# Kernel optimization log

Measured on AMD Instinct MI355X. Metric: run time of the kernel, lower is better.

## Reference

```python
import jax, jax.numpy as jnp
import numpy as np


def setup_inputs() -> dict:
    key = jax.random.key(0)
    k1, = jax.random.split(key, 1)
    b, l, h, w, c = 2, 16, 16, 16, 32
    inputs = jax.random.normal(k1, (b, l, h, w, c), dtype=jnp.float32)
    gamma = jnp.ones((1,), dtype=jnp.float32)
    return {"inputs": inputs, "gamma": gamma}


def reference(inputs, gamma):
    b, l, h, w, c = inputs.shape
    n = l * h * w
    # torch: x = permute->view gives [b, c, n]; here keep [b, n, c] (same memory layout of values)
    xr = inputs.reshape(b, n, c)
    # scores[b,i,j] = sum_c x[b,c,i] * x[b,c,j]
    scores = jnp.einsum('bic,bjc->bij', xr, xr)
    attn = jax.nn.softmax(scores, axis=-1)  # softmax over j (dim=-1)
    # out[b,c,j] = sum_i x[b,c,i] * attn[b,i,j]  ->  [b, n, c] layout
    out = jnp.einsum('bic,bij->bjc', xr, attn)
    out = out.reshape(b, l, h, w, c)
    return out * gamma + inputs
```

## Files before the change

### kernel.cpp

```cpp
#include <hip/hip_runtime.h>


typedef _Float16 half8 __attribute__((ext_vector_type(8)));
typedef _Float16 half4v __attribute__((ext_vector_type(4)));
typedef _Float16 half2v __attribute__((ext_vector_type(2)));
typedef float float4v __attribute__((ext_vector_type(4)));
typedef int int4v __attribute__((ext_vector_type(4)));

#define NN 4096
#define CC 32
#define L2E 1.44269504f
#define SHIFT 48.0f

__global__ __launch_bounds__(256) void k_convert(const float* __restrict__ x,
                                                 _Float16* __restrict__ xf,
                                                 _Float16* __restrict__ xt) {
    const int t = blockIdx.x * 256 + threadIdx.x;
    const int n  = t & 4095;
    const int cg = (t >> 12) & 7;
    const int b  = t >> 15;
    const int row = (b << 12) | n;
    const float4* src = (const float4*)(x + (size_t)row * CC + cg * 4);
    float4 v = *src;
    _Float16 h0 = (_Float16)v.x, h1 = (_Float16)v.y, h2 = (_Float16)v.z, h3 = (_Float16)v.w;
    *(half4v*)(xf + (size_t)row * CC + cg * 4) = (half4v){h0, h1, h2, h3};
    _Float16* xtb = xt + (size_t)b * CC * NN;
    xtb[(cg * 4 + 0) * NN + n] = h0;
    xtb[(cg * 4 + 1) * NN + n] = h1;
    xtb[(cg * 4 + 2) * NN + n] = h2;
    xtb[(cg * 4 + 3) * NN + n] = h3;
}

__global__ __launch_bounds__(512, 2) void k_pass1(const _Float16* __restrict__ xf,
                                                  float* __restrict__ c2out) {
    const int tid = threadIdx.x;
    const int wave = tid >> 6, lane = tid & 63;
    const int quad = lane >> 4, l15 = lane & 15;
    const int b = blockIdx.x >> 7;
    const int i0 = (blockIdx.x & 127) * 32;
    const _Float16* xb = xf + (size_t)b * NN * CC;

    const half8 af0 = *(const half8*)(xb + (size_t)(i0 + l15) * CC + quad * 8);
    const half8 af1 = *(const half8*)(xb + (size_t)(i0 + 16 + l15) * CC + quad * 8);
    const float4v zf = {0.f, 0.f, 0.f, 0.f};
    float z0[4] = {0.f, 0.f, 0.f, 0.f};
    float z1[4] = {0.f, 0.f, 0.f, 0.f};
    const float c2c = -SHIFT * L2E;

    const int jbase = wave * 512;
    half8 b0 = *(const half8*)(xb + (size_t)(jbase + l15) * CC + quad * 8);
    half8 b1 = *(const half8*)(xb + (size_t)(jbase + 16 + l15) * CC + quad * 8);
    half8 b2 = *(const half8*)(xb + (size_t)(jbase + 32 + l15) * CC + quad * 8);
    half8 b3 = *(const half8*)(xb + (size_t)(jbase + 48 + l15) * CC + quad * 8);

    for (int jt = 0; jt < 8; ++jt) {
        const int jn = jbase + ((jt + 1) & 7) * 64;
        half8 n0 = *(const half8*)(xb + (size_t)(jn + l15) * CC + quad * 8);
        half8 n1 = *(const half8*)(xb + (size_t)(jn + 16 + l15) * CC + quad * 8);
        half8 n2 = *(const half8*)(xb + (size_t)(jn + 32 + l15) * CC + quad * 8);
        half8 n3 = *(const half8*)(xb + (size_t)(jn + 48 + l15) * CC + quad * 8);

        float4v s00 = __builtin_amdgcn_mfma_f32_16x16x32_f16(af0, b0, zf, 0, 0, 0);
        float4v s01 = __builtin_amdgcn_mfma_f32_16x16x32_f16(af0, b1, zf, 0, 0, 0);
        float4v s02 = __builtin_amdgcn_mfma_f32_16x16x32_f16(af0, b2, zf, 0, 0, 0);
        float4v s03 = __builtin_amdgcn_mfma_f32_16x16x32_f16(af0, b3, zf, 0, 0, 0);
        float4v s10 = __builtin_amdgcn_mfma_f32_16x16x32_f16(af1, b0, zf, 0, 0, 0);
        float4v s11 = __builtin_amdgcn_mfma_f32_16x16x32_f16(af1, b1, zf, 0, 0, 0);
        float4v s12 = __builtin_amdgcn_mfma_f32_16x16x32_f16(af1, b2, zf, 0, 0, 0);
        float4v s13 = __builtin_amdgcn_mfma_f32_16x16x32_f16(af1, b3, zf, 0, 0, 0);
#pragma unroll
        for (int r = 0; r < 4; ++r) {
            z0[r] += __builtin_amdgcn_exp2f(fmaf(s00[r], L2E, c2c));
            z0[r] += __builtin_amdgcn_exp2f(fmaf(s01[r], L2E, c2c));
            z0[r] += __builtin_amdgcn_exp2f(fmaf(s02[r], L2E, c2c));
            z0[r] += __builtin_amdgcn_exp2f(fmaf(s03[r], L2E, c2c));
            z1[r] += __builtin_amdgcn_exp2f(fmaf(s10[r], L2E, c2c));
            z1[r] += __builtin_amdgcn_exp2f(fmaf(s11[r], L2E, c2c));
            z1[r] += __builtin_amdgcn_exp2f(fmaf(s12[r], L2E, c2c));
            z1[r] += __builtin_amdgcn_exp2f(fmaf(s13[r], L2E, c2c));
        }
        b0 = n0; b1 = n1; b2 = n2; b3 = n3;
    }
#pragma unroll
    for (int off = 1; off <= 8; off <<= 1) {
#pragma unroll
        for (int r = 0; r < 4; ++r) {
            z0[r] += __shfl_xor(z0[r], off, 64);
            z1[r] += __shfl_xor(z1[r], off, 64);
        }
    }
    __shared__ float zw[8][32];
    if (l15 == 0) {
#pragma unroll
        for (int r = 0; r < 4; ++r) {
            zw[wave][quad * 4 + r]      = z0[r];
            zw[wave][16 + quad * 4 + r] = z1[r];
        }
    }
    __syncthreads();
    if (tid < 32) {
        float zs = 0.f;
#pragma unroll
        for (int w = 0; w < 8; ++w) zs += zw[w][tid];
        c2out[b * NN + i0 + tid] = -(__builtin_amdgcn_logf(zs) + SHIFT * L2E);
    }
}

__global__ __launch_bounds__(512, 2) void k_pass2(const _Float16* __restrict__ xf,
                                                  const _Float16* __restrict__ xt,
                                                  const float* __restrict__ c2,
                                                  const float* __restrict__ x,
                                                  const float* __restrict__ gamma,
                                                  float* __restrict__ out) {
    const int tid = threadIdx.x;
    const int wave = tid >> 6, lane = tid & 63;
    const int quad = lane >> 4, l15 = lane & 15;
    const int b = blockIdx.x >> 7;
    const int j0 = (blockIdx.x & 127) * 32;
    const _Float16* xb  = xf + (size_t)b * NN * CC;
    const _Float16* xtb = xt + (size_t)b * CC * NN;
    const float* c2b = c2 + b * NN;

    __shared__ float red[8][32][32];

    const int addrLo = (((quad & 1) << 5) + l15) << 2;
    const int addrHi = addrLo + 64;
    const bool lo32 = (lane < 32);

    const half8 bj0 = *(const half8*)(xb + (size_t)(j0 + l15) * CC + quad * 8);
    const half8 bj1 = *(const half8*)(xb + (size_t)(j0 + 16 + l15) * CC + quad * 8);
    const float4v zf = {0.f, 0.f, 0.f, 0.f};
    float4v acc00 = zf, acc01 = zf, acc10 = zf, acc11 = zf;

    const int ibase = wave * 512;
    half8 a0  = *(const half8*)(xb + (size_t)(ibase + l15) * CC + quad * 8);
    half8 a1  = *(const half8*)(xb + (size_t)(ibase + 16 + l15) * CC + quad * 8);
    half8 xb0 = *(const half8*)(xtb + (size_t)l15 * NN + ibase + quad * 8);
    half8 xb1 = *(const half8*)(xtb + (size_t)(l15 + 16) * NN + ibase + quad * 8);
    float4v c20 = *(const float4v*)(c2b + ibase + quad * 4);
    float4v c21 = *(const float4v*)(c2b + ibase + 16 + quad * 4);

    for (int it = 0; it < 16; ++it) {
        const int inx = ibase + ((it + 1) & 15) * 32;
        half8 na0  = *(const half8*)(xb + (size_t)(inx + l15) * CC + quad * 8);
        half8 na1  = *(const half8*)(xb + (size_t)(inx + 16 + l15) * CC + quad * 8);
        half8 nxb0 = *(const half8*)(xtb + (size_t)l15 * NN + inx + quad * 8);
        half8 nxb1 = *(const half8*)(xtb + (size_t)(l15 + 16) * NN + inx + quad * 8);
        float4v nc20 = *(const float4v*)(c2b + inx + quad * 4);
        float4v nc21 = *(const float4v*)(c2b + inx + 16 + quad * 4);

        float4v s00 = __builtin_amdgcn_mfma_f32_16x16x32_f16(a0, bj0, zf, 0, 0, 0);
        float4v s10 = __builtin_amdgcn_mfma_f32_16x16x32_f16(a1, bj0, zf, 0, 0, 0);
        float4v s01 = __builtin_amdgcn_mfma_f32_16x16x32_f16(a0, bj1, zf, 0, 0, 0);
        float4v s11 = __builtin_amdgcn_mfma_f32_16x16x32_f16(a1, bj1, zf, 0, 0, 0);
        float4v e00, e10, e01, e11;
#pragma unroll
        for (int r = 0; r < 4; ++r) {
            e00[r] = __builtin_amdgcn_exp2f(fmaf(s00[r], L2E, c20[r]));
            e10[r] = __builtin_amdgcn_exp2f(fmaf(s10[r], L2E, c21[r]));
            e01[r] = __builtin_amdgcn_exp2f(fmaf(s01[r], L2E, c20[r]));
            e11[r] = __builtin_amdgcn_exp2f(fmaf(s11[r], L2E, c21[r]));
        }
        {
            const int d0 = __builtin_bit_cast(int, (half2v)__builtin_amdgcn_cvt_pkrtz(e00[0], e00[1]));
            const int d1 = __builtin_bit_cast(int, (half2v)__builtin_amdgcn_cvt_pkrtz(e00[2], e00[3]));
            const int d2 = __builtin_bit_cast(int, (half2v)__builtin_amdgcn_cvt_pkrtz(e10[0], e10[1]));
            const int d3 = __builtin_bit_cast(int, (half2v)__builtin_amdgcn_cvt_pkrtz(e10[2], e10[3]));
            const int q0 = __builtin_amdgcn_ds_bpermute(addrLo, d0);
            const int q1 = __builtin_amdgcn_ds_bpermute(addrLo, d1);
            const int q2 = __builtin_amdgcn_ds_bpermute(addrHi, d0);
            const int q3 = __builtin_amdgcn_ds_bpermute(addrHi, d1);
            const int q4 = __builtin_amdgcn_ds_bpermute(addrLo, d2);
            const int q5 = __builtin_amdgcn_ds_bpermute(addrLo, d3);
            const int q6 = __builtin_amdgcn_ds_bpermute(addrHi, d2);
            const int q7 = __builtin_amdgcn_ds_bpermute(addrHi, d3);
            int4v ai;
            ai[0] = lo32 ? q0 : q4;
            ai[1] = lo32 ? q1 : q5;
            ai[2] = lo32 ? q2 : q6;
            ai[3] = lo32 ? q3 : q7;
            const half8 a2 = __builtin_bit_cast(half8, ai);
            acc00 = __builtin_amdgcn_mfma_f32_16x16x32_f16(a2, xb0, acc00, 0, 0, 0);
            acc01 = __builtin_amdgcn_mfma_f32_16x16x32_f16(a2, xb1, acc01, 0, 0, 0);
        }
        {
            const int d0 = __builtin_bit_cast(int, (half2v)__builtin_amdgcn_cvt_pkrtz(e01[0], e01[1]));
            const int d1 = __builtin_bit_cast(int, (half2v)__builtin_amdgcn_cvt_pkrtz(e01[2], e01[3]));
            const int d2 = __builtin_bit_cast(int, (half2v)__builtin_amdgcn_cvt_pkrtz(e11[0], e11[1]));
            const int d3 = __builtin_bit_cast(int, (half2v)__builtin_amdgcn_cvt_pkrtz(e11[2], e11[3]));
            const int q0 = __builtin_amdgcn_ds_bpermute(addrLo, d0);
            const int q1 = __builtin_amdgcn_ds_bpermute(addrLo, d1);
            const int q2 = __builtin_amdgcn_ds_bpermute(addrHi, d0);
            const int q3 = __builtin_amdgcn_ds_bpermute(addrHi, d1);
            const int q4 = __builtin_amdgcn_ds_bpermute(addrLo, d2);
            const int q5 = __builtin_amdgcn_ds_bpermute(addrLo, d3);
            const int q6 = __builtin_amdgcn_ds_bpermute(addrHi, d2);
            const int q7 = __builtin_amdgcn_ds_bpermute(addrHi, d3);
            int4v ai;
            ai[0] = lo32 ? q0 : q4;
            ai[1] = lo32 ? q1 : q5;
            ai[2] = lo32 ? q2 : q6;
            ai[3] = lo32 ? q3 : q7;
            const half8 a2 = __builtin_bit_cast(half8, ai);
            acc10 = __builtin_amdgcn_mfma_f32_16x16x32_f16(a2, xb0, acc10, 0, 0, 0);
            acc11 = __builtin_amdgcn_mfma_f32_16x16x32_f16(a2, xb1, acc11, 0, 0, 0);
        }

        a0 = na0; a1 = na1; xb0 = nxb0; xb1 = nxb1; c20 = nc20; c21 = nc21;
    }

#pragma unroll
    for (int r = 0; r < 4; ++r) {
        red[wave][quad * 4 + r][l15]           = acc00[r];
        red[wave][quad * 4 + r][l15 + 16]      = acc01[r];
        red[wave][16 + quad * 4 + r][l15]      = acc10[r];
        red[wave][16 + quad * 4 + r][l15 + 16] = acc11[r];
    }
    __syncthreads();
    {
        const int jj = tid >> 5, c = tid & 31;
        const float g = gamma[0];
#pragma unroll
        for (int h = 0; h < 2; ++h) {
            const int j = jj + h * 16;
            float s = 0.f;
#pragma unroll
            for (int w = 0; w < 8; ++w) s += red[w][j][c];
            const size_t o = (size_t)(b * NN + j0 + j) * CC + c;
            out[o] = fmaf(g, s, x[o]);
        }
    }
}

extern "C" void kernel_launch(void* const* d_in, const int* in_sizes, int n_in,
                              void* d_out, int out_size, void* d_ws, size_t ws_size,
                              hipStream_t stream) {
    const float* x     = (const float*)d_in[0];
    const float* gamma = (const float*)d_in[1];
    float* out = (float*)d_out;

    _Float16* xf = (_Float16*)d_ws;
    _Float16* xt = xf + (size_t)2 * NN * CC;
    float*    c2 = (float*)(xt + (size_t)2 * CC * NN);

    k_convert<<<dim3(256), dim3(256), 0, stream>>>(x, xf, xt);
    k_pass1 <<<dim3(256), dim3(512), 0, stream>>>(xf, c2);
    k_pass2 <<<dim3(256), dim3(512), 0, stream>>>(xf, xt, c2, x, gamma, out);
}
```

Measured before the change: 79.65 us.

## Double per-block query tile to 64 rows and tile transposed copy for contiguous loads

Both attention passes now process 64 rows/columns per block instead of 32, so each loaded key/value fragment is reused across twice as many MFMA tiles, and the grid drops from 256 to 128 blocks. The transposed fp16 copy is re-laid out in 32-position chunks so each lane's 8-element load in pass 2 is contiguous within a small tile rather than strided by N. The trade-off is fewer blocks than compute units on a 256-CU device, more registers and more shared memory (64 KB reduction buffer) per block, which may reduce occupancy.

```diff
diff --git a/kernel.cpp b/kernel.cpp
--- a/kernel.cpp
+++ b/kernel.cpp
@@ -24,11 +24,11 @@
     float4 v = *src;
     _Float16 h0 = (_Float16)v.x, h1 = (_Float16)v.y, h2 = (_Float16)v.z, h3 = (_Float16)v.w;
     *(half4v*)(xf + (size_t)row * CC + cg * 4) = (half4v){h0, h1, h2, h3};
-    _Float16* xtb = xt + (size_t)b * CC * NN;
-    xtb[(cg * 4 + 0) * NN + n] = h0;
-    xtb[(cg * 4 + 1) * NN + n] = h1;
-    xtb[(cg * 4 + 2) * NN + n] = h2;
-    xtb[(cg * 4 + 3) * NN + n] = h3;
+    _Float16* p = xt + (size_t)b * CC * NN + (size_t)(n >> 5) * (CC * 32) + cg * 4 * 32 + (n & 31);
+    p[0]  = h0;
+    p[32] = h1;
+    p[64] = h2;
+    p[96] = h3;
 }
 
 __global__ __launch_bounds__(512, 2) void k_pass1(const _Float16* __restrict__ xf,
@@ -36,15 +36,19 @@
     const int tid = threadIdx.x;
     const int wave = tid >> 6, lane = tid & 63;
     const int quad = lane >> 4, l15 = lane & 15;
-    const int b = blockIdx.x >> 7;
-    const int i0 = (blockIdx.x & 127) * 32;
+    const int b = blockIdx.x >> 6;
+    const int i0 = (blockIdx.x & 63) * 64;
     const _Float16* xb = xf + (size_t)b * NN * CC;
 
     const half8 af0 = *(const half8*)(xb + (size_t)(i0 + l15) * CC + quad * 8);
     const half8 af1 = *(const half8*)(xb + (size_t)(i0 + 16 + l15) * CC + quad * 8);
+    const half8 af2 = *(const half8*)(xb + (size_t)(i0 + 32 + l15) * CC + quad * 8);
+    const half8 af3 = *(const half8*)(xb + (size_t)(i0 + 48 + l15) * CC + quad * 8);
     const float4v zf = {0.f, 0.f, 0.f, 0.f};
     float z0[4] = {0.f, 0.f, 0.f, 0.f};
     float z1[4] = {0.f, 0.f, 0.f, 0.f};
+    float z2[4] = {0.f, 0.f, 0.f, 0.f};
+    float z3[4] = {0.f, 0.f, 0.f, 0.f};
     const float c2c = -SHIFT * L2E;
 
     const int jbase = wave * 512;
@@ -60,24 +64,47 @@
         half8 n2 = *(const half8*)(xb + (size_t)(jn + 32 + l15) * CC + quad * 8);
         half8 n3 = *(const half8*)(xb + (size_t)(jn + 48 + l15) * CC + quad * 8);
 
-        float4v s00 = __builtin_amdgcn_mfma_f32_16x16x32_f16(af0, b0, zf, 0, 0, 0);
-        float4v s01 = __builtin_amdgcn_mfma_f32_16x16x32_f16(af0, b1, zf, 0, 0, 0);
-        float4v s02 = __builtin_amdgcn_mfma_f32_16x16x32_f16(af0, b2, zf, 0, 0, 0);
-        float4v s03 = __builtin_amdgcn_mfma_f32_16x16x32_f16(af0, b3, zf, 0, 0, 0);
-        float4v s10 = __builtin_amdgcn_mfma_f32_16x16x32_f16(af1, b0, zf, 0, 0, 0);
-        float4v s11 = __builtin_amdgcn_mfma_f32_16x16x32_f16(af1, b1, zf, 0, 0, 0);
-        float4v s12 = __builtin_amdgcn_mfma_f32_16x16x32_f16(af1, b2, zf, 0, 0, 0);
-        float4v s13 = __builtin_amdgcn_mfma_f32_16x16x32_f16(af1, b3, zf, 0, 0, 0);
-#pragma unroll
-        for (int r = 0; r < 4; ++r) {
-            z0[r] += __builtin_amdgcn_exp2f(fmaf(s00[r], L2E, c2c));
-            z0[r] += __builtin_amdgcn_exp2f(fmaf(s01[r], L2E, c2c));
-            z0[r] += __builtin_amdgcn_exp2f(fmaf(s02[r], L2E, c2c));
-            z0[r] += __builtin_amdgcn_exp2f(fmaf(s03[r], L2E, c2c));
-            z1[r] += __builtin_amdgcn_exp2f(fmaf(s10[r], L2E, c2c));
-            z1[r] += __builtin_amdgcn_exp2f(fmaf(s11[r], L2E, c2c));
-            z1[r] += __builtin_amdgcn_exp2f(fmaf(s12[r], L2E, c2c));
-            z1[r] += __builtin_amdgcn_exp2f(fmaf(s13[r], L2E, c2c));
+        {
+            float4v s00 = __builtin_amdgcn_mfma_f32_16x16x32_f16(af0, b0, zf, 0, 0, 0);
+            float4v s01 = __builtin_amdgcn_mfma_f32_16x16x32_f16(af0, b1, zf, 0, 0, 0);
+            float4v s02 = __builtin_amdgcn_mfma_f32_16x16x32_f16(af0, b2, zf, 0, 0, 0);
+            float4v s03 = __builtin_amdgcn_mfma_f32_16x16x32_f16(af0, b3, zf, 0, 0, 0);
+            float4v s10 = __builtin_amdgcn_mfma_f32_16x16x32_f16(af1, b0, zf, 0, 0, 0);
+            float4v s11 = __builtin_amdgcn_mfma_f32_16x16x32_f16(af1, b1, zf, 0, 0, 0);
+            float4v s12 = __builtin_amdgcn_mfma_f32_16x16x32_f16(af1, b2, zf, 0, 0, 0);
+            float4v s13 = __builtin_amdgcn_mfma_f32_16x16x32_f16(af1, b3, zf, 0, 0, 0);
+#pragma unroll
+            for (int r = 0; r < 4; ++r) {
+                z0[r] += __builtin_amdgcn_exp2f(fmaf(s00[r], L2E, c2c));
+                z0[r] += __builtin_amdgcn_exp2f(fmaf(s01[r], L2E, c2c));
+                z0[r] += __builtin_amdgcn_exp2f(fmaf(s02[r], L2E, c2c));
+                z0[r] += __builtin_amdgcn_exp2f(fmaf(s03[r], L2E, c2c));
+                z1[r] += __builtin_amdgcn_exp2f(fmaf(s10[r], L2E, c2c));
+                z1[r] += __builtin_amdgcn_exp2f(fmaf(s11[r], L2E, c2c));
+                z1[r] += __builtin_amdgcn_exp2f(fmaf(s12[r], L2E, c2c));
+                z1[r] += __builtin_amdgcn_exp2f(fmaf(s13[r], L2E, c2c));
+            }
+        }
+        {
+            float4v s00 = __builtin_amdgcn_mfma_f32_16x16x32_f16(af2, b0, zf, 0, 0, 0);
+            float4v s01 = __builtin_amdgcn_mfma_f32_16x16x32_f16(af2, b1, zf, 0, 0, 0);
+            float4v s02 = __builtin_amdgcn_mfma_f32_16x16x32_f16(af2, b2, zf, 0, 0, 0);
+            float4v s03 = __builtin_amdgcn_mfma_f32_16x16x32_f16(af2, b3, zf, 0, 0, 0);
+            float4v s10 = __builtin_amdgcn_mfma_f32_16x16x32_f16(af3, b0, zf, 0, 0, 0);
+            float4v s11 = __builtin_amdgcn_mfma_f32_16x16x32_f16(af3, b1, zf, 0, 0, 0);
+            float4v s12 = __builtin_amdgcn_mfma_f32_16x16x32_f16(af3, b2, zf, 0, 0, 0);
+            float4v s13 = __builtin_amdgcn_mfma_f32_16x16x32_f16(af3, b3, zf, 0, 0, 0);
+#pragma unroll
+            for (int r = 0; r < 4; ++r) {
+                z2[r] += __builtin_amdgcn_exp2f(fmaf(s00[r], L2E, c2c));
+                z2[r] += __builtin_amdgcn_exp2f(fmaf(s01[r], L2E, c2c));
+                z2[r] += __builtin_amdgcn_exp2f(fmaf(s02[r], L2E, c2c));
+                z2[r] += __builtin_amdgcn_exp2f(fmaf(s03[r], L2E, c2c));
+                z3[r] += __builtin_amdgcn_exp2f(fmaf(s10[r], L2E, c2c));
+                z3[r] += __builtin_amdgcn_exp2f(fmaf(s11[r], L2E, c2c));
+                z3[r] += __builtin_amdgcn_exp2f(fmaf(s12[r], L2E, c2c));
+                z3[r] += __builtin_amdgcn_exp2f(fmaf(s13[r], L2E, c2c));
+            }
         }
         b0 = n0; b1 = n1; b2 = n2; b3 = n3;
     }
@@ -87,18 +114,22 @@
         for (int r = 0; r < 4; ++r) {
             z0[r] += __shfl_xor(z0[r], off, 64);
             z1[r] += __shfl_xor(z1[r], off, 64);
-        }
-    }
-    __shared__ float zw[8][32];
+            z2[r] += __shfl_xor(z2[r], off, 64);
+            z3[r] += __shfl_xor(z3[r], off, 64);
+        }
+    }
+    __shared__ float zw[8][64];
     if (l15 == 0) {
 #pragma unroll
         for (int r = 0; r < 4; ++r) {
             zw[wave][quad * 4 + r]      = z0[r];
             zw[wave][16 + quad * 4 + r] = z1[r];
+            zw[wave][32 + quad * 4 + r] = z2[r];
+            zw[wave][48 + quad * 4 + r] = z3[r];
         }
     }
     __syncthreads();
-    if (tid < 32) {
+    if (tid < 64) {
         float zs = 0.f;
 #pragma unroll
         for (int w = 0; w < 8; ++w) zs += zw[w][tid];
@@ -115,13 +146,13 @@
     const int tid = threadIdx.x;
     const int wave = tid >> 6, lane = tid & 63;
     const int quad = lane >> 4, l15 = lane & 15;
-    const int b = blockIdx.x >> 7;
-    const int j0 = (blockIdx.x & 127) * 32;
+    const int b = blockIdx.x >> 6;
+    const int j0 = (blockIdx.x & 63) * 64;
     const _Float16* xb  = xf + (size_t)b * NN * CC;
     const _Float16* xtb = xt + (size_t)b * CC * NN;
     const float* c2b = c2 + b * NN;
 
-    __shared__ float red[8][32][32];
+    __shared__ float red[8][64][32];
 
     const int addrLo = (((quad & 1) << 5) + l15) << 2;
     const int addrHi = addrLo + 64;
@@ -129,14 +160,17 @@
 
     const half8 bj0 = *(const half8*)(xb + (size_t)(j0 + l15) * CC + quad * 8);
     const half8 bj1 = *(const half8*)(xb + (size_t)(j0 + 16 + l15) * CC + quad * 8);
+    const half8 bj2 = *(const half8*)(xb + (size_t)(j0 + 32 + l15) * CC + quad * 8);
+    const half8 bj3 = *(const half8*)(xb + (size_t)(j0 + 48 + l15) * CC + quad * 8);
     const float4v zf = {0.f, 0.f, 0.f, 0.f};
     float4v acc00 = zf, acc01 = zf, acc10 = zf, acc11 = zf;
+    float4v acc20 = zf, acc21 = zf, acc30 = zf, acc31 = zf;
 
     const int ibase = wave * 512;
     half8 a0  = *(const half8*)(xb + (size_t)(ibase + l15) * CC + quad * 8);
     half8 a1  = *(const half8*)(xb + (size_t)(ibase + 16 + l15) * CC + quad * 8);
-    half8 xb0 = *(const half8*)(xtb + (size_t)l15 * NN + ibase + quad * 8);
-    half8 xb1 = *(const half8*)(xtb + (size_t)(l15 + 16) * NN + ibase + quad * 8);
+    half8 xb0 = *(const half8*)(xtb + (size_t)ibase * 32 + l15 * 32 + quad * 8);
+    half8 xb1 = *(const half8*)(xtb + (size_t)ibase * 32 + 512 + l15 * 32 + quad * 8);
     float4v c20 = *(const float4v*)(c2b + ibase + quad * 4);
     float4v c21 = *(const float4v*)(c2b + ibase + 16 + quad * 4);
 
@@ -144,66 +178,126 @@
         const int inx = ibase + ((it + 1) & 15) * 32;
         half8 na0  = *(const half8*)(xb + (size_t)(inx + l15) * CC + quad * 8);
         half8 na1  = *(const half8*)(xb + (size_t)(inx + 16 + l15) * CC + quad * 8);
-        half8 nxb0 = *(const half8*)(xtb + (size_t)l15 * NN + inx + quad * 8);
-        half8 nxb1 = *(const half8*)(xtb + (size_t)(l15 + 16) * NN + inx + quad * 8);
+        half8 nxb0 = *(const half8*)(xtb + (size_t)inx * 32 + l15 * 32 + quad * 8);
+        half8 nxb1 = *(const half8*)(xtb + (size_t)inx * 32 + 512 + l15 * 32 + quad * 8);
         float4v nc20 = *(const float4v*)(c2b + inx + quad * 4);
         float4v nc21 = *(const float4v*)(c2b + inx + 16 + quad * 4);
 
-        float4v s00 = __builtin_amdgcn_mfma_f32_16x16x32_f16(a0, bj0, zf, 0, 0, 0);
-        float4v s10 = __builtin_amdgcn_mfma_f32_16x16x32_f16(a1, bj0, zf, 0, 0, 0);
-        float4v s01 = __builtin_amdgcn_mfma_f32_16x16x32_f16(a0, bj1, zf, 0, 0, 0);
-        float4v s11 = __builtin_amdgcn_mfma_f32_16x16x32_f16(a1, bj1, zf, 0, 0, 0);
-        float4v e00, e10, e01, e11;
-#pragma unroll
-        for (int r = 0; r < 4; ++r) {
-            e00[r] = __builtin_amdgcn_exp2f(fmaf(s00[r], L2E, c20[r]));
-            e10[r] = __builtin_amdgcn_exp2f(fmaf(s10[r], L2E, c21[r]));
-            e01[r] = __builtin_amdgcn_exp2f(fmaf(s01[r], L2E, c20[r]));
-            e11[r] = __builtin_amdgcn_exp2f(fmaf(s11[r], L2E, c21[r]));
-        }
         {
-            const int d0 = __builtin_bit_cast(int, (half2v)__builtin_amdgcn_cvt_pkrtz(e00[0], e00[1]));
-            const int d1 = __builtin_bit_cast(int, (half2v)__builtin_amdgcn_cvt_pkrtz(e00[2], e00[3]));
-            const int d2 = __builtin_bit_cast(int, (half2v)__builtin_amdgcn_cvt_pkrtz(e10[0], e10[1]));
-            const int d3 = __builtin_bit_cast(int, (half2v)__builtin_amdgcn_cvt_pkrtz(e10[2], e10[3]));
-            const int q0 = __builtin_amdgcn_ds_bpermute(addrLo, d0);
-            const int q1 = __builtin_amdgcn_ds_bpermute(addrLo, d1);
-            const int q2 = __builtin_amdgcn_ds_bpermute(addrHi, d0);
-            const int q3 = __builtin_amdgcn_ds_bpermute(addrHi, d1);
-            const int q4 = __builtin_amdgcn_ds_bpermute(addrLo, d2);
-            const int q5 = __builtin_amdgcn_ds_bpermute(addrLo, d3);
-            const int q6 = __builtin_amdgcn_ds_bpermute(addrHi, d2);
-            const int q7 = __builtin_amdgcn_ds_bpermute(addrHi, d3);
-            int4v ai;
-            ai[0] = lo32 ? q0 : q4;
-            ai[1] = lo32 ? q1 : q5;
-            ai[2] = lo32 ? q2 : q6;
-            ai[3] = lo32 ? q3 : q7;
-            const half8 a2 = __builtin_bit_cast(half8, ai);
-            acc00 = __builtin_amdgcn_mfma_f32_16x16x32_f16(a2, xb0, acc00, 0, 0, 0);
-            acc01 = __builtin_amdgcn_mfma_f32_16x16x32_f16(a2, xb1, acc01, 0, 0, 0);
+            float4v s00 = __builtin_amdgcn_mfma_f32_16x16x32_f16(a0, bj0, zf, 0, 0, 0);
+            float4v s10 = __builtin_amdgcn_mfma_f32_16x16x32_f16(a1, bj0, zf, 0, 0, 0);
+            float4v s01 = __builtin_amdgcn_mfma_f32_16x16x32_f16(a0, bj1, zf, 0, 0, 0);
+            float4v s11 = __builtin_amdgcn_mfma_f32_16x16x32_f16(a1, bj1, zf, 0, 0, 0);
+            float4v e00, e10, e01, e11;
+#pragma unroll
+            for (int r = 0; r < 4; ++r) {
+                e00[r] = __builtin_amdgcn_exp2f(fmaf(s00[r], L2E, c20[r]));
+                e10[r] = __builtin_amdgcn_exp2f(fmaf(s10[r], L2E, c21[r]));
+                e01[r] = __builtin_amdgcn_exp2f(fmaf(s01[r], L2E, c20[r]));
+                e11[r] = __builtin_amdgcn_exp2f(fmaf(s11[r], L2E, c21[r]));
+            }
+            {
+                const int d0 = __builtin_bit_cast(int, (half2v)__builtin_amdgcn_cvt_pkrtz(e00[0], e00[1]));
+                const int d1 = __builtin_bit_cast(int, (half2v)__builtin_amdgcn_cvt_pkrtz(e00[2], e00[3]));
+                const int d2 = __builtin_bit_cast(int, (half2v)__builtin_amdgcn_cvt_pkrtz(e10[0], e10[1]));
+                const int d3 = __builtin_bit_cast(int, (half2v)__builtin_amdgcn_cvt_pkrtz(e10[2], e10[3]));
+                const int q0 = __builtin_amdgcn_ds_bpermute(addrLo, d0);
+                const int q1 = __builtin_amdgcn_ds_bpermute(addrLo, d1);
+                const int q2 = __builtin_amdgcn_ds_bpermute(addrHi, d0);
+                const int q3 = __builtin_amdgcn_ds_bpermute(addrHi, d1);
+                const int q4 = __builtin_amdgcn_ds_bpermute(addrLo, d2);
+                const int q5 = __builtin_amdgcn_ds_bpermute(addrLo, d3);
+                const int q6 = __builtin_amdgcn_ds_bpermute(addrHi, d2);
+                const int q7 = __builtin_amdgcn_ds_bpermute(addrHi, d3);
+                int4v ai;
+                ai[0] = lo32 ? q0 : q4;
+                ai[1] = lo32 ? q1 : q5;
+                ai[2] = lo32 ? q2 : q6;
+                ai[3] = lo32 ? q3 : q7;
+                const half8 a2 = __builtin_bit_cast(half8, ai);
+                acc00 = __builtin_amdgcn_mfma_f32_16x16x32_f16(a2, xb0, acc00, 0, 0, 0);
+                acc01 = __builtin_amdgcn_mfma_f32_16x16x32_f16(a2, xb1, acc01, 0, 0, 0);
+            }
+            {
+                const int d0 = __builtin_bit_cast(int, (half2v)__builtin_amdgcn_cvt_pkrtz(e01[0], e01[1]));
+                const int d1 = __builtin_bit_cast(int, (half2v)__builtin_amdgcn_cvt_pkrtz(e01[2], e01[3]));
+                const int d2 = __builtin_bit_cast(int, (half2v)__builtin_amdgcn_cvt_pkrtz(e11[0], e11[1]));
+                const int d3 = __builtin_bit_cast(int, (half2v)__builtin_amdgcn_cvt_pkrtz(e11[2], e11[3]));
+                const int q0 = __builtin_amdgcn_ds_bpermute(addrLo, d0);
+                const int q1 = __builtin_amdgcn_ds_bpermute(addrLo, d1);
+                const int q2 = __builtin_amdgcn_ds_bpermute(addrHi, d0);
+                const int q3 = __builtin_amdgcn_ds_bpermute(addrHi, d1);
+                const int q4 = __builtin_amdgcn_ds_bpermute(addrLo, d2);
+                const int q5 = __builtin_amdgcn_ds_bpermute(addrLo, d3);
+                const int q6 = __builtin_amdgcn_ds_bpermute(addrHi, d2);
+                const int q7 = __builtin_amdgcn_ds_bpermute(addrHi, d3);
+                int4v ai;
+                ai[0] = lo32 ? q0 : q4;
+                ai[1] = lo32 ? q1 : q5;
+                ai[2] = lo32 ? q2 : q6;
+                ai[3] = lo32 ? q3 : q7;
+                const half8 a2 = __builtin_bit_cast(half8, ai);
+                acc10 = __builtin_amdgcn_mfma_f32_16x16x32_f16(a2, xb0, acc10, 0, 0, 0);
+                acc11 = __builtin_amdgcn_mfma_f32_16x16x32_f16(a2, xb1, acc11, 0, 0, 0);
+            }
         }
         {
-            const int d0 = __builtin_bit_cast(int, (half2v)__builtin_amdgcn_cvt_pkrtz(e01[0], e01[1]));
-            const int d1 = __builtin_bit_cast(int, (half2v)__builtin_amdgcn_cvt_pkrtz(e01[2], e01[3]));
-            const int d2 = __builtin_bit_cast(int, (half2v)__builtin_amdgcn_cvt_pkrtz(e11[0], e11[1]));
-            const int d3 = __builtin_bit_cast(int, (half2v)__builtin_amdgcn_cvt_pkrtz(e11[2], e11[3]));
-            const int q0 = __builtin_amdgcn_ds_bpermute(addrLo, d0);
-            const int q1 = __builtin_amdgcn_ds_bpermute(addrLo, d1);
-            const int q2 = __builtin_amdgcn_ds_bpermute(addrHi, d0);
-            const int q3 = __builtin_amdgcn_ds_bpermute(addrHi, d1);
-            const int q4 = __builtin_amdgcn_ds_bpermute(addrLo, d2);
-            const int q5 = __builtin_amdgcn_ds_bpermute(addrLo, d3);
-            const int q6 = __builtin_amdgcn_ds_bpermute(addrHi, d2);
-            const int q7 = __builtin_amdgcn_ds_bpermute(addrHi, d3);
-            int4v ai;
-            ai[0] = lo32 ? q0 : q4;
-            ai[1] = lo32 ? q1 : q5;
-            ai[2] = lo32 ? q2 : q6;
-            ai[3] = lo32 ? q3 : q7;
-            const half8 a2 = __builtin_bit_cast(half8, ai);
-            acc10 = __builtin_amdgcn_mfma_f32_16x16x32_f16(a2, xb0, acc10, 0, 0, 0);
-            acc11 = __builtin_amdgcn_mfma_f32_16x16x32_f16(a2, xb1, acc11, 0, 0, 0);
+            float4v s00 = __builtin_amdgcn_mfma_f32_16x16x32_f16(a0, bj2, zf, 0, 0, 0);
+            float4v s10 = __builtin_amdgcn_mfma_f32_16x16x32_f16(a1, bj2, zf, 0, 0, 0);
+            float4v s01 = __builtin_amdgcn_mfma_f32_16x16x32_f16(a0, bj3, zf, 0, 0, 0);
+            float4v s11 = __builtin_amdgcn_mfma_f32_16x16x32_f16(a1, bj3, zf, 0, 0, 0);
+            float4v e00, e10, e01, e11;
+#pragma unroll
+            for (int r = 0; r < 4; ++r) {
+                e00[r] = __builtin_amdgcn_exp2f(fmaf(s00[r], L2E, c20[r]));
+                e10[r] = __builtin_amdgcn_exp2f(fmaf(s10[r], L2E, c21[r]));
+                e01[r] = __builtin_amdgcn_exp2f(fmaf(s01[r], L2E, c20[r]));
+                e11[r] = __builtin_amdgcn_exp2f(fmaf(s11[r], L2E, c21[r]));
+            }
+            {
+                const int d0 = __builtin_bit_cast(int, (half2v)__builtin_amdgcn_cvt_pkrtz(e00[0], e00[1]));
+                const int d1 = __builtin_bit_cast(int, (half2v)__builtin_amdgcn_cvt_pkrtz(e00[2], e00[3]));
+                const int d2 = __builtin_bit_cast(int, (half2v)__builtin_amdgcn_cvt_pkrtz(e10[0], e10[1]));
+                const int d3 = __builtin_bit_cast(int, (half2v)__builtin_amdgcn_cvt_pkrtz(e10[2], e10[3]));
+                const int q0 = __builtin_amdgcn_ds_bpermute(addrLo, d0);
+                const int q1 = __builtin_amdgcn_ds_bpermute(addrLo, d1);
+                const int q2 = __builtin_amdgcn_ds_bpermute(addrHi, d0);
+                const int q3 = __builtin_amdgcn_ds_bpermute(addrHi, d1);
+                const int q4 = __builtin_amdgcn_ds_bpermute(addrLo, d2);
+                const int q5 = __builtin_amdgcn_ds_bpermute(addrLo, d3);
+                const int q6 = __builtin_amdgcn_ds_bpermute(addrHi, d2);
+                const int q7 = __builtin_amdgcn_ds_bpermute(addrHi, d3);
+                int4v ai;
+                ai[0] = lo32 ? q0 : q4;
+                ai[1] = lo32 ? q1 : q5;
+                ai[2] = lo32 ? q2 : q6;
+                ai[3] = lo32 ? q3 : q7;
+                const half8 a2 = __builtin_bit_cast(half8, ai);
+                acc20 = __builtin_amdgcn_mfma_f32_16x16x32_f16(a2, xb0, acc20, 0, 0, 0);
+                acc21 = __builtin_amdgcn_mfma_f32_16x16x32_f16(a2, xb1, acc21, 0, 0, 0);
+            }
+            {
+                const int d0 = __builtin_bit_cast(int, (half2v)__builtin_amdgcn_cvt_pkrtz(e01[0], e01[1]));
+                const int d1 = __builtin_bit_cast(int, (half2v)__builtin_amdgcn_cvt_pkrtz(e01[2], e01[3]));
+                const int d2 = __builtin_bit_cast(int, (half2v)__builtin_amdgcn_cvt_pkrtz(e11[0], e11[1]));
+                const int d3 = __builtin_bit_cast(int, (half2v)__builtin_amdgcn_cvt_pkrtz(e11[2], e11[3]));
+                const int q0 = __builtin_amdgcn_ds_bpermute(addrLo, d0);
+                const int q1 = __builtin_amdgcn_ds_bpermute(addrLo, d1);
+                const int q2 = __builtin_amdgcn_ds_bpermute(addrHi, d0);
+                const int q3 = __builtin_amdgcn_ds_bpermute(addrHi, d1);
+                const int q4 = __builtin_amdgcn_ds_bpermute(addrLo, d2);
+                const int q5 = __builtin_amdgcn_ds_bpermute(addrLo, d3);
+                const int q6 = __builtin_amdgcn_ds_bpermute(addrHi, d2);
+                const int q7 = __builtin_amdgcn_ds_bpermute(addrHi, d3);
+                int4v ai;
+                ai[0] = lo32 ? q0 : q4;
+                ai[1] = lo32 ? q1 : q5;
+                ai[2] = lo32 ? q2 : q6;
+                ai[3] = lo32 ? q3 : q7;
+                const half8 a2 = __builtin_bit_cast(half8, ai);
+                acc30 = __builtin_amdgcn_mfma_f32_16x16x32_f16(a2, xb0, acc30, 0, 0, 0);
+                acc31 = __builtin_amdgcn_mfma_f32_16x16x32_f16(a2, xb1, acc31, 0, 0, 0);
+            }
         }
 
         a0 = na0; a1 = na1; xb0 = nxb0; xb1 = nxb1; c20 = nc20; c21 = nc21;
@@ -215,13 +309,17 @@
         red[wave][quad * 4 + r][l15 + 16]      = acc01[r];
         red[wave][16 + quad * 4 + r][l15]      = acc10[r];
         red[wave][16 + quad * 4 + r][l15 + 16] = acc11[r];
+        red[wave][32 + quad * 4 + r][l15]      = acc20[r];
+        red[wave][32 + quad * 4 + r][l15 + 16] = acc21[r];
+        red[wave][48 + quad * 4 + r][l15]      = acc30[r];
+        red[wave][48 + quad * 4 + r][l15 + 16] = acc31[r];
     }
     __syncthreads();
     {
         const int jj = tid >> 5, c = tid & 31;
         const float g = gamma[0];
 #pragma unroll
-        for (int h = 0; h < 2; ++h) {
+        for (int h = 0; h < 4; ++h) {
             const int j = jj + h * 16;
             float s = 0.f;
 #pragma unroll
@@ -244,6 +342,6 @@
     float*    c2 = (float*)(xt + (size_t)2 * CC * NN);
 
     k_convert<<<dim3(256), dim3(256), 0, stream>>>(x, xf, xt);
-    k_pass1 <<<dim3(256), dim3(512), 0, stream>>>(xf, c2);
-    k_pass2 <<<dim3(256), dim3(512), 0, stream>>>(xf, xt, c2, x, gamma, out);
+    k_pass1 <<<dim3(128), dim3(512), 0, stream>>>(xf, c2);
+    k_pass2 <<<dim3(128), dim3(512), 0, stream>>>(xf, xt, c2, x, gamma, out);
 }
```

Result: slower. 87.49 us (+9.9%).

## Retile softmax-denominator pass into 2D blocks with atomic partial sums

Applied to the files above, without the earlier changes.

Pass 1 now gives each block a 512x256 tile of the score matrix, and each wave owns 64 rows instead of the block sharing 32 rows. Per-wave partial exp sums are accumulated into a global buffer with atomicAdd, which removes the shared-memory reduction and barrier. The buffer is zeroed in the convert kernel, and the log moves into pass 2, which recomputes it per loaded element. The aim is more A-operand reuse per B load and less per-block synchronisation. In exchange it adds atomics, extra log work in pass 2's inner loop and more register pressure.

```diff
diff --git a/kernel.cpp b/kernel.cpp
--- a/kernel.cpp
+++ b/kernel.cpp
@@ -14,7 +14,8 @@
 
 __global__ __launch_bounds__(256) void k_convert(const float* __restrict__ x,
                                                  _Float16* __restrict__ xf,
-                                                 _Float16* __restrict__ xt) {
+                                                 _Float16* __restrict__ xt,
+                                                 float* __restrict__ zbuf) {
     const int t = blockIdx.x * 256 + threadIdx.x;
     const int n  = t & 4095;
     const int cg = (t >> 12) & 7;
@@ -29,55 +30,86 @@
     xtb[(cg * 4 + 1) * NN + n] = h1;
     xtb[(cg * 4 + 2) * NN + n] = h2;
     xtb[(cg * 4 + 3) * NN + n] = h3;
+    if (t < 2 * NN) zbuf[t] = 0.f;
 }
 
 __global__ __launch_bounds__(512, 2) void k_pass1(const _Float16* __restrict__ xf,
-                                                  float* __restrict__ c2out) {
+                                                  float* __restrict__ zbuf) {
     const int tid = threadIdx.x;
     const int wave = tid >> 6, lane = tid & 63;
     const int quad = lane >> 4, l15 = lane & 15;
     const int b = blockIdx.x >> 7;
-    const int i0 = (blockIdx.x & 127) * 32;
+    const int r7 = blockIdx.x & 127;
+    const int I0 = (r7 >> 4) * 512;
+    const int J0 = (r7 & 15) * 256;
     const _Float16* xb = xf + (size_t)b * NN * CC;
-
-    const half8 af0 = *(const half8*)(xb + (size_t)(i0 + l15) * CC + quad * 8);
-    const half8 af1 = *(const half8*)(xb + (size_t)(i0 + 16 + l15) * CC + quad * 8);
+    float* zb = zbuf + b * NN;
+
+    const int ib = I0 + wave * 64;
+    const half8 af0 = *(const half8*)(xb + (size_t)(ib + l15) * CC + quad * 8);
+    const half8 af1 = *(const half8*)(xb + (size_t)(ib + 16 + l15) * CC + quad * 8);
+    const half8 af2 = *(const half8*)(xb + (size_t)(ib + 32 + l15) * CC + quad * 8);
+    const half8 af3 = *(const half8*)(xb + (size_t)(ib + 48 + l15) * CC + quad * 8);
     const float4v zf = {0.f, 0.f, 0.f, 0.f};
     float z0[4] = {0.f, 0.f, 0.f, 0.f};
     float z1[4] = {0.f, 0.f, 0.f, 0.f};
+    float z2[4] = {0.f, 0.f, 0.f, 0.f};
+    float z3[4] = {0.f, 0.f, 0.f, 0.f};
     const float c2c = -SHIFT * L2E;
 
-    const int jbase = wave * 512;
-    half8 b0 = *(const half8*)(xb + (size_t)(jbase + l15) * CC + quad * 8);
-    half8 b1 = *(const half8*)(xb + (size_t)(jbase + 16 + l15) * CC + quad * 8);
-    half8 b2 = *(const half8*)(xb + (size_t)(jbase + 32 + l15) * CC + quad * 8);
-    half8 b3 = *(const half8*)(xb + (size_t)(jbase + 48 + l15) * CC + quad * 8);
-
-    for (int jt = 0; jt < 8; ++jt) {
-        const int jn = jbase + ((jt + 1) & 7) * 64;
+    half8 b0 = *(const half8*)(xb + (size_t)(J0 + l15) * CC + quad * 8);
+    half8 b1 = *(const half8*)(xb + (size_t)(J0 + 16 + l15) * CC + quad * 8);
+    half8 b2 = *(const half8*)(xb + (size_t)(J0 + 32 + l15) * CC + quad * 8);
+    half8 b3 = *(const half8*)(xb + (size_t)(J0 + 48 + l15) * CC + quad * 8);
+
+    for (int jt = 0; jt < 4; ++jt) {
+        const int jn = J0 + ((jt + 1) & 3) * 64;
         half8 n0 = *(const half8*)(xb + (size_t)(jn + l15) * CC + quad * 8);
         half8 n1 = *(const half8*)(xb + (size_t)(jn + 16 + l15) * CC + quad * 8);
         half8 n2 = *(const half8*)(xb + (size_t)(jn + 32 + l15) * CC + quad * 8);
         half8 n3 = *(const half8*)(xb + (size_t)(jn + 48 + l15) * CC + quad * 8);
 
-        float4v s00 = __builtin_amdgcn_mfma_f32_16x16x32_f16(af0, b0, zf, 0, 0, 0);
-        float4v s01 = __builtin_amdgcn_mfma_f32_16x16x32_f16(af0, b1, zf, 0, 0, 0);
-        float4v s02 = __builtin_amdgcn_mfma_f32_16x16x32_f16(af0, b2, zf, 0, 0, 0);
-        float4v s03 = __builtin_amdgcn_mfma_f32_16x16x32_f16(af0, b3, zf, 0, 0, 0);
-        float4v s10 = __builtin_amdgcn_mfma_f32_16x16x32_f16(af1, b0, zf, 0, 0, 0);
-        float4v s11 = __builtin_amdgcn_mfma_f32_16x16x32_f16(af1, b1, zf, 0, 0, 0);
-        float4v s12 = __builtin_amdgcn_mfma_f32_16x16x32_f16(af1, b2, zf, 0, 0, 0);
-        float4v s13 = __builtin_amdgcn_mfma_f32_16x16x32_f16(af1, b3, zf, 0, 0, 0);
-#pragma unroll
-        for (int r = 0; r < 4; ++r) {
-            z0[r] += __builtin_amdgcn_exp2f(fmaf(s00[r], L2E, c2c));
-            z0[r] += __builtin_amdgcn_exp2f(fmaf(s01[r], L2E, c2c));
-            z0[r] += __builtin_amdgcn_exp2f(fmaf(s02[r], L2E, c2c));
-            z0[r] += __builtin_amdgcn_exp2f(fmaf(s03[r], L2E, c2c));
-            z1[r] += __builtin_amdgcn_exp2f(fmaf(s10[r], L2E, c2c));
-            z1[r] += __builtin_amdgcn_exp2f(fmaf(s11[r], L2E, c2c));
-            z1[r] += __builtin_amdgcn_exp2f(fmaf(s12[r], L2E, c2c));
-            z1[r] += __builtin_amdgcn_exp2f(fmaf(s13[r], L2E, c2c));
+        {
+            float4v s00 = __builtin_amdgcn_mfma_f32_16x16x32_f16(af0, b0, zf, 0, 0, 0);
+            float4v s01 = __builtin_amdgcn_mfma_f32_16x16x32_f16(af0, b1, zf, 0, 0, 0);
+            float4v s02 = __builtin_amdgcn_mfma_f32_16x16x32_f16(af0, b2, zf, 0, 0, 0);
+            float4v s03 = __builtin_amdgcn_mfma_f32_16x16x32_f16(af0, b3, zf, 0, 0, 0);
+            float4v s10 = __builtin_amdgcn_mfma_f32_16x16x32_f16(af1, b0, zf, 0, 0, 0);
+            float4v s11 = __builtin_amdgcn_mfma_f32_16x16x32_f16(af1, b1, zf, 0, 0, 0);
+            float4v s12 = __builtin_amdgcn_mfma_f32_16x16x32_f16(af1, b2, zf, 0, 0, 0);
+            float4v s13 = __builtin_amdgcn_mfma_f32_16x16x32_f16(af1, b3, zf, 0, 0, 0);
+#pragma unroll
+            for (int r = 0; r < 4; ++r) {
+                z0[r] += __builtin_amdgcn_exp2f(fmaf(s00[r], L2E, c2c));
+                z0[r] += __builtin_amdgcn_exp2f(fmaf(s01[r], L2E, c2c));
+                z0[r] += __builtin_amdgcn_exp2f(fmaf(s02[r], L2E, c2c));
+                z0[r] += __builtin_amdgcn_exp2f(fmaf(s03[r], L2E, c2c));
+                z1[r] += __builtin_amdgcn_exp2f(fmaf(s10[r], L2E, c2c));
+                z1[r] += __builtin_amdgcn_exp2f(fmaf(s11[r], L2E, c2c));
+                z1[r] += __builtin_amdgcn_exp2f(fmaf(s12[r], L2E, c2c));
+                z1[r] += __builtin_amdgcn_exp2f(fmaf(s13[r], L2E, c2c));
+            }
+        }
+        {
+            float4v s00 = __builtin_amdgcn_mfma_f32_16x16x32_f16(af2, b0, zf, 0, 0, 0);
+            float4v s01 = __builtin_amdgcn_mfma_f32_16x16x32_f16(af2, b1, zf, 0, 0, 0);
+            float4v s02 = __builtin_amdgcn_mfma_f32_16x16x32_f16(af2, b2, zf, 0, 0, 0);
+            float4v s03 = __builtin_amdgcn_mfma_f32_16x16x32_f16(af2, b3, zf, 0, 0, 0);
+            float4v s10 = __builtin_amdgcn_mfma_f32_16x16x32_f16(af3, b0, zf, 0, 0, 0);
+            float4v s11 = __builtin_amdgcn_mfma_f32_16x16x32_f16(af3, b1, zf, 0, 0, 0);
+            float4v s12 = __builtin_amdgcn_mfma_f32_16x16x32_f16(af3, b2, zf, 0, 0, 0);
+            float4v s13 = __builtin_amdgcn_mfma_f32_16x16x32_f16(af3, b3, zf, 0, 0, 0);
+#pragma unroll
+            for (int r = 0; r < 4; ++r) {
+                z2[r] += __builtin_amdgcn_exp2f(fmaf(s00[r], L2E, c2c));
+                z2[r] += __builtin_amdgcn_exp2f(fmaf(s01[r], L2E, c2c));
+                z2[r] += __builtin_amdgcn_exp2f(fmaf(s02[r], L2E, c2c));
+                z2[r] += __builtin_amdgcn_exp2f(fmaf(s03[r], L2E, c2c));
+                z3[r] += __builtin_amdgcn_exp2f(fmaf(s10[r], L2E, c2c));
+                z3[r] += __builtin_amdgcn_exp2f(fmaf(s11[r], L2E, c2c));
+                z3[r] += __builtin_amdgcn_exp2f(fmaf(s12[r], L2E, c2c));
+                z3[r] += __builtin_amdgcn_exp2f(fmaf(s13[r], L2E, c2c));
+            }
         }
         b0 = n0; b1 = n1; b2 = n2; b3 = n3;
     }
@@ -87,28 +119,24 @@
         for (int r = 0; r < 4; ++r) {
             z0[r] += __shfl_xor(z0[r], off, 64);
             z1[r] += __shfl_xor(z1[r], off, 64);
-        }
-    }
-    __shared__ float zw[8][32];
+            z2[r] += __shfl_xor(z2[r], off, 64);
+            z3[r] += __shfl_xor(z3[r], off, 64);
+        }
+    }
     if (l15 == 0) {
 #pragma unroll
         for (int r = 0; r < 4; ++r) {
-            zw[wave][quad * 4 + r]      = z0[r];
-            zw[wave][16 + quad * 4 + r] = z1[r];
-        }
-    }
-    __syncthreads();
-    if (tid < 32) {
-        float zs = 0.f;
-#pragma unroll
-        for (int w = 0; w < 8; ++w) zs += zw[w][tid];
-        c2out[b * NN + i0 + tid] = -(__builtin_amdgcn_logf(zs) + SHIFT * L2E);
+            atomicAdd(&zb[ib + quad * 4 + r],      z0[r]);
+            atomicAdd(&zb[ib + 16 + quad * 4 + r], z1[r]);
+            atomicAdd(&zb[ib + 32 + quad * 4 + r], z2[r]);
+            atomicAdd(&zb[ib + 48 + quad * 4 + r], z3[r]);
+        }
     }
 }
 
 __global__ __launch_bounds__(512, 2) void k_pass2(const _Float16* __restrict__ xf,
                                                   const _Float16* __restrict__ xt,
-                                                  const float* __restrict__ c2,
+                                                  const float* __restrict__ zbuf,
                                                   const float* __restrict__ x,
                                                   const float* __restrict__ gamma,
                                                   float* __restrict__ out) {
@@ -119,7 +147,7 @@
     const int j0 = (blockIdx.x & 127) * 32;
     const _Float16* xb  = xf + (size_t)b * NN * CC;
     const _Float16* xtb = xt + (size_t)b * CC * NN;
-    const float* c2b = c2 + b * NN;
+    const float* zb = zbuf + b * NN;
 
     __shared__ float red[8][32][32];
 
@@ -137,8 +165,16 @@
     half8 a1  = *(const half8*)(xb + (size_t)(ibase + 16 + l15) * CC + quad * 8);
     half8 xb0 = *(const half8*)(xtb + (size_t)l15 * NN + ibase + quad * 8);
     half8 xb1 = *(const half8*)(xtb + (size_t)(l15 + 16) * NN + ibase + quad * 8);
-    float4v c20 = *(const float4v*)(c2b + ibase + quad * 4);
-    float4v c21 = *(const float4v*)(c2b + ibase + 16 + quad * 4);
+    float4v c20, c21;
+    {
+        float4v zz0 = *(const float4v*)(zb + ibase + quad * 4);
+        float4v zz1 = *(const float4v*)(zb + ibase + 16 + quad * 4);
+#pragma unroll
+        for (int r = 0; r < 4; ++r) {
+            c20[r] = -(__builtin_amdgcn_logf(zz0[r]) + SHIFT * L2E);
+            c21[r] = -(__builtin_amdgcn_logf(zz1[r]) + SHIFT * L2E);
+        }
+    }
 
     for (int it = 0; it < 16; ++it) {
         const int inx = ibase + ((it + 1) & 15) * 32;
@@ -146,8 +182,8 @@
         half8 na1  = *(const half8*)(xb + (size_t)(inx + 16 + l15) * CC + quad * 8);
         half8 nxb0 = *(const half8*)(xtb + (size_t)l15 * NN + inx + quad * 8);
         half8 nxb1 = *(const half8*)(xtb + (size_t)(l15 + 16) * NN + inx + quad * 8);
-        float4v nc20 = *(const float4v*)(c2b + inx + quad * 4);
-        float4v nc21 = *(const float4v*)(c2b + inx + 16 + quad * 4);
+        float4v nzz0 = *(const float4v*)(zb + inx + quad * 4);
+        float4v nzz1 = *(const float4v*)(zb + inx + 16 + quad * 4);
 
         float4v s00 = __builtin_amdgcn_mfma_f32_16x16x32_f16(a0, bj0, zf, 0, 0, 0);
         float4v s10 = __builtin_amdgcn_mfma_f32_16x16x32_f16(a1, bj0, zf, 0, 0, 0);
@@ -206,7 +242,12 @@
             acc11 = __builtin_amdgcn_mfma_f32_16x16x32_f16(a2, xb1, acc11, 0, 0, 0);
         }
 
-        a0 = na0; a1 = na1; xb0 = nxb0; xb1 = nxb1; c20 = nc20; c21 = nc21;
+        a0 = na0; a1 = na1; xb0 = nxb0; xb1 = nxb1;
+#pragma unroll
+        for (int r = 0; r < 4; ++r) {
+            c20[r] = -(__builtin_amdgcn_logf(nzz0[r]) + SHIFT * L2E);
+            c21[r] = -(__builtin_amdgcn_logf(nzz1[r]) + SHIFT * L2E);
+        }
     }
 
 #pragma unroll
@@ -241,9 +282,9 @@
 
     _Float16* xf = (_Float16*)d_ws;
     _Float16* xt = xf + (size_t)2 * NN * CC;
-    float*    c2 = (float*)(xt + (size_t)2 * CC * NN);
-
-    k_convert<<<dim3(256), dim3(256), 0, stream>>>(x, xf, xt);
-    k_pass1 <<<dim3(256), dim3(512), 0, stream>>>(xf, c2);
-    k_pass2 <<<dim3(256), dim3(512), 0, stream>>>(xf, xt, c2, x, gamma, out);
-}
+    float*    zbuf = (float*)(xt + (size_t)2 * CC * NN);
+
+    k_convert<<<dim3(256), dim3(256), 0, stream>>>(x, xf, xt, zbuf);
+    k_pass1 <<<dim3(256), dim3(512), 0, stream>>>(xf, zbuf);
+    k_pass2 <<<dim3(256), dim3(512), 0, stream>>>(xf, xt, zbuf, x, gamma, out);
+}
```

Result: slower. 84.59 us (+6.2%).
